# Optimization experiments

Measured on AMD Instinct MI355X. Metric: run time of the kernel, lower is better.

## Reference

```python
import jax, jax.numpy as jnp
import numpy as np

B, N, D = 32, 2048, 128
NUM_QUERIES = 16
K_FRAC = 0.5
NUM_SUPPORTS = N - NUM_QUERIES
K_KEEP = int(K_FRAC * NUM_SUPPORTS)  # 1016
M = K_KEEP + NUM_QUERIES             # pooled node count, 1032


def setup_inputs() -> dict:
    key = jax.random.key(0)
    k1, k2, k3 = jax.random.split(key, 3)
    A = jax.random.normal(k1, (B, N, N), dtype=jnp.float32)
    X = jax.random.normal(k2, (B, N, D), dtype=jnp.float32)
    w = jax.random.normal(k3, (D,), dtype=jnp.float32) * 0.1  # proj weight (out_dim=1)
    b = jnp.zeros((1,), dtype=jnp.float32)                     # proj bias
    return {"A": A, "X": X, "w": w, "b": b}


def reference(A, X, w, b):
    # per-node scores: sigmoid(Linear(X)/100), shape [B, N]
    scores = jax.nn.sigmoid((jnp.einsum('bnd,d->bn', X, w) + b[0]) / 100.0)
    support_scores = scores[:, :NUM_SUPPORTS]                     # [B, S]
    intra = support_scores - support_scores.mean(axis=1, keepdims=True)
    # torch.topk(largest=False) == top_k of negated values (ascending order)
    _, support_idx = jax.lax.top_k(-intra, K_KEEP)                # [B, K]
    support_values = jnp.take_along_axis(support_scores, support_idx, axis=1)
    query_idx = jnp.broadcast_to(jnp.arange(NUM_SUPPORTS, N, dtype=support_idx.dtype), (B, NUM_QUERIES))
    query_values = scores[:, NUM_SUPPORTS:]
    idx = jnp.concatenate([support_idx, query_idx], axis=1)       # [B, M]
    values = jnp.concatenate([support_values, query_values], axis=1)  # [B, M]
    # gather + scale node features
    new_X = jnp.take_along_axis(X, idx[:, :, None], axis=1) * values[:, :, None]  # [B, M, D]
    # double gather on adjacency: A[i, idx][:, idx]
    rows = jnp.take_along_axis(A, idx[:, :, None], axis=1)        # [B, M, N]
    new_A = jnp.take_along_axis(rows, idx[:, None, :], axis=2)    # [B, M, M]
    return (new_A, new_X, idx)
```

## Files before the change

kernel.cpp:

```cpp
#include <hip/hip_runtime.h>

#define NB 32
#define NN 2048
#define ND 128
#define NSUP 2032
#define KKEEP 1016
#define MM 1032
#define SEG 254

typedef unsigned long long u64;
typedef unsigned int u32;
typedef float f32x4 __attribute__((ext_vector_type(4)));

__device__ __forceinline__ float mulrn(float a, float b) {
  float r;
  asm("v_mul_f32 %0, %1, %2" : "=v"(r) : "v"(a), "v"(b));
  return r;
}
__device__ __forceinline__ float addrn(float a, float b) {
  float r;
  asm("v_add_f32 %0, %1, %2" : "=v"(r) : "v"(a), "v"(b));
  return r;
}
__device__ __forceinline__ float fmarn(float a, float b, float c) {
  float r;
  asm("v_fma_f32 %0, %1, %2, %3" : "=v"(r) : "v"(a), "v"(b), "v"(c));
  return r;
}

__global__ __launch_bounds__(256) void k_score(const float* __restrict__ X,
                                               const float* __restrict__ w,
                                               const float* __restrict__ bias,
                                               u64* __restrict__ keys,
                                               float* __restrict__ score) {
#pragma clang fp contract(off)
  int row = blockIdx.x * 256 + threadIdx.x;
  if (row >= NB * NN) return;
  const float* x = X + (size_t)row * ND;

  float l[16];
  #pragma unroll
  for (int k = 0; k < 16; ++k) l[k] = 0.f;
  #pragma unroll
  for (int step = 0; step < 8; ++step) {
    const float* xp = x + step * 16;
    const float* wp = w + step * 16;
    #pragma unroll
    for (int q4 = 0; q4 < 4; ++q4) {
      const float4 xv = *reinterpret_cast<const float4*>(xp + q4 * 4);
      const float4 wv = *reinterpret_cast<const float4*>(wp + q4 * 4);
      l[q4 * 4 + 0] = addrn(mulrn(xv.x, wv.x), l[q4 * 4 + 0]);
      l[q4 * 4 + 1] = addrn(mulrn(xv.y, wv.y), l[q4 * 4 + 1]);
      l[q4 * 4 + 2] = addrn(mulrn(xv.z, wv.z), l[q4 * 4 + 2]);
      l[q4 * 4 + 3] = addrn(mulrn(xv.w, wv.w), l[q4 * 4 + 3]);
    }
  }
  #pragma unroll
  for (int k = 0; k < 8; ++k) l[k] = addrn(l[k], l[k + 8]);
  #pragma unroll
  for (int k = 0; k < 4; ++k) l[k] = addrn(l[k], l[k + 4]);
  l[0] = addrn(l[0], l[2]);
  l[1] = addrn(l[1], l[3]);
  const float dot = addrn(l[0], l[1]);

  const float z = __fdiv_rn(addrn(dot, bias[0]), 100.0f);

  const float xe = -z;
  const float z2 = mulrn(xe, xe);
  float y = fmarn(1.9875691500E-4f, xe, 1.3981999507E-3f);
  y = fmarn(y, xe, 8.3334519073E-3f);
  y = fmarn(y, xe, 4.1665795894E-2f);
  y = fmarn(y, xe, 1.6666665459E-1f);
  y = fmarn(y, xe, 5.0000001201E-1f);
  y = fmarn(y, z2, xe);
  const float e = addrn(y, 1.0f);

  const float s = __fdiv_rn(1.0f, addrn(1.0f, e));

  score[row] = s;

  const u32 sb = __float_as_uint(s);
  const int n = row & (NN - 1);
  keys[row] = ((u64)sb << 32) | (u32)n;
}

__global__ __launch_bounds__(256) void k_rank(const u64* __restrict__ keys,
                                              const float* __restrict__ score,
                                              int* __restrict__ idxs,
                                              float* __restrict__ vals,
                                              float* __restrict__ out_idx) {
  __shared__ u64 lk[NSUP];
  const int b   = blockIdx.x >> 3;
  const int seg = blockIdx.x & 7;
  const int t   = threadIdx.x;
  const size_t bNN = (size_t)b * NN;
  const int    bMM = b * MM;

  for (int i = t; i < NSUP; i += 256) lk[i] = keys[bNN + i];
  __syncthreads();

  if (t < SEG) {
    const int e  = seg * SEG + t;
    const u64 my = lk[e];
    int cnt = 0;
    #pragma unroll 4
    for (int s = 0; s < NSUP; s += 4) {
      const u64 k0 = lk[s], k1 = lk[s + 1], k2 = lk[s + 2], k3 = lk[s + 3];
      cnt += (int)(k0 < my) + (int)(k1 < my) + (int)(k2 < my) + (int)(k3 < my);
    }
    if (cnt < KKEEP) {
      idxs[bMM + cnt]    = e;
      vals[bMM + cnt]    = score[bNN + e];
      out_idx[bMM + cnt] = (float)e;
    }
  } else {
    const int q   = seg * 2 + (t - SEG);
    const int e   = NSUP + q;
    const int pos = KKEEP + q;
    idxs[bMM + pos]    = e;
    vals[bMM + pos]    = score[bNN + e];
    out_idx[bMM + pos] = (float)e;
  }
}

__global__ __launch_bounds__(128) void k_newa(const float* __restrict__ A,
                                              const float* __restrict__ X,
                                              const int* __restrict__ idxs,
                                              const float* __restrict__ vals,
                                              float* __restrict__ out_a,
                                              float* __restrict__ out_x) {
  __shared__ float srow[NN];
  __shared__ int   scols[MM];
  int row = blockIdx.x;
  int b   = row / MM;
  const int* cols = idxs + b * MM;
  for (int c = threadIdx.x; c < MM / 4; c += 128)
    *reinterpret_cast<int4*>(&scols[c * 4]) =
        reinterpret_cast<const int4*>(cols)[c];

  int ri = idxs[row];
  const float* arow = A + ((size_t)b * NN + ri) * NN;
  #pragma unroll
  for (int i = 0; i < 4; ++i) {
    int off = (threadIdx.x + i * 128) * 4;
    *reinterpret_cast<f32x4*>(&srow[off]) =
        __builtin_nontemporal_load(reinterpret_cast<const f32x4*>(arow + off));
  }

  if (threadIdx.x < 32) {
    float v = vals[row];
    const float4 xv = reinterpret_cast<const float4*>(
        X + ((size_t)b * NN + ri) * ND)[threadIdx.x];
    float4 o = make_float4(xv.x * v, xv.y * v, xv.z * v, xv.w * v);
    reinterpret_cast<float4*>(out_x + (size_t)row * ND)[threadIdx.x] = o;
  }
  __syncthreads();

  f32x4* orow = reinterpret_cast<f32x4*>(out_a + (size_t)row * MM);
  for (int c = threadIdx.x; c < MM / 4; c += 128) {
    const int4 j4 = *reinterpret_cast<const int4*>(scols + c * 4);
    f32x4 o;
    o.x = srow[j4.x];
    o.y = srow[j4.y];
    o.z = srow[j4.z];
    o.w = srow[j4.w];
    __builtin_nontemporal_store(o, orow + c);
  }
}

extern "C" void kernel_launch(void* const* d_in, const int* in_sizes, int n_in,
                              void* d_out, int out_size, void* d_ws, size_t ws_size,
                              hipStream_t stream) {
  const float* A    = (const float*)d_in[0];
  const float* X    = (const float*)d_in[1];
  const float* w    = (const float*)d_in[2];
  const float* bias = (const float*)d_in[3];

  float* out0 = (float*)d_out;
  float* out1 = out0 + (size_t)NB * MM * MM;
  float* out2 = out1 + (size_t)NB * MM * ND;

  u64*   keys  = (u64*)d_ws;
  float* score = (float*)(keys + NB * NN);
  int*   idxs  = (int*)(score + NB * NN);
  float* vals  = (float*)(idxs + NB * MM);

  hipLaunchKernelGGL(k_score, dim3(NB * NN / 256), dim3(256), 0, stream, X, w, bias, keys, score);
  hipLaunchKernelGGL(k_rank,  dim3(NB * 8),        dim3(256), 0, stream, keys, score, idxs, vals, out2);
  hipLaunchKernelGGL(k_newa,  dim3(NB * MM),       dim3(128), 0, stream, A, X, idxs, vals, out0, out1);
}
```

Baseline: 109.8 us.

## Process multiple rows per block in k_newa with double-buffered row prefetch

The gather kernel now handles 12 output rows per 256-thread block instead of one row per 128-thread block. The column index table is loaded once per block and reused across those rows. The next source row of A is prefetched into registers while the current row is gathered from shared memory, with double-buffered LDS. This amortises per-block setup and overlaps the global load latency with the gather and store, at the cost of fewer blocks (2752) and two barriers per row.

After: 129.7 us. 1.18x slower.

```diff
diff --git a/kernel.cpp b/kernel.cpp
--- a/kernel.cpp
+++ b/kernel.cpp
@@ -7,6 +7,7 @@
 #define KKEEP 1016
 #define MM 1032
 #define SEG 254
+#define RPB 12
 
 typedef unsigned long long u64;
 typedef unsigned int u32;
@@ -123,48 +124,73 @@
   }
 }
 
-__global__ __launch_bounds__(128) void k_newa(const float* __restrict__ A,
+__global__ __launch_bounds__(256) void k_newa(const float* __restrict__ A,
                                               const float* __restrict__ X,
                                               const int* __restrict__ idxs,
                                               const float* __restrict__ vals,
                                               float* __restrict__ out_a,
                                               float* __restrict__ out_x) {
-  __shared__ float srow[NN];
+  __shared__ float buf[2][NN];
   __shared__ int   scols[MM];
-  int row = blockIdx.x;
-  int b   = row / MM;
+  const int t     = threadIdx.x;
+  const int b     = blockIdx.x / (MM / RPB);
+  const int chunk = blockIdx.x % (MM / RPB);
+  const int row0  = b * MM + chunk * RPB;
   const int* cols = idxs + b * MM;
-  for (int c = threadIdx.x; c < MM / 4; c += 128)
+  const float* Ab = A + (size_t)b * NN * NN;
+  const float* Xb = X + (size_t)b * NN * ND;
+
+  for (int c = t; c < MM / 4; c += 256)
     *reinterpret_cast<int4*>(&scols[c * 4]) =
         reinterpret_cast<const int4*>(cols)[c];
 
-  int ri = idxs[row];
-  const float* arow = A + ((size_t)b * NN + ri) * NN;
-  #pragma unroll
-  for (int i = 0; i < 4; ++i) {
-    int off = (threadIdx.x + i * 128) * 4;
-    *reinterpret_cast<f32x4*>(&srow[off]) =
-        __builtin_nontemporal_load(reinterpret_cast<const f32x4*>(arow + off));
-  }
-
-  if (threadIdx.x < 32) {
-    float v = vals[row];
-    const float4 xv = reinterpret_cast<const float4*>(
-        X + ((size_t)b * NN + ri) * ND)[threadIdx.x];
-    float4 o = make_float4(xv.x * v, xv.y * v, xv.z * v, xv.w * v);
-    reinterpret_cast<float4*>(out_x + (size_t)row * ND)[threadIdx.x] = o;
-  }
+  f32x4 r0, r1;
+  {
+    const f32x4* ar = reinterpret_cast<const f32x4*>(Ab + (size_t)idxs[row0] * NN);
+    r0 = __builtin_nontemporal_load(ar + t);
+    r1 = __builtin_nontemporal_load(ar + 256 + t);
+  }
+  reinterpret_cast<f32x4*>(buf[0])[t]       = r0;
+  reinterpret_cast<f32x4*>(buf[0])[256 + t] = r1;
   __syncthreads();
 
-  f32x4* orow = reinterpret_cast<f32x4*>(out_a + (size_t)row * MM);
-  for (int c = threadIdx.x; c < MM / 4; c += 128) {
-    const int4 j4 = *reinterpret_cast<const int4*>(scols + c * 4);
-    f32x4 o;
-    o.x = srow[j4.x];
-    o.y = srow[j4.y];
-    o.z = srow[j4.z];
-    o.w = srow[j4.w];
-    __builtin_nontemporal_store(o, orow + c);
+  int cur = 0;
+  for (int r = 0; r < RPB; ++r) {
+    const int row = row0 + r;
+    const bool more = (r + 1 < RPB);
+    if (more) {
+      const f32x4* ar = reinterpret_cast<const f32x4*>(
+          Ab + (size_t)idxs[row + 1] * NN);
+      r0 = __builtin_nontemporal_load(ar + t);
+      r1 = __builtin_nontemporal_load(ar + 256 + t);
+    }
+
+    if (t < 32) {
+      const float v = vals[row];
+      const float4 xv = reinterpret_cast<const float4*>(
+          Xb + (size_t)idxs[row] * ND)[t];
+      float4 o = make_float4(xv.x * v, xv.y * v, xv.z * v, xv.w * v);
+      reinterpret_cast<float4*>(out_x + (size_t)row * ND)[t] = o;
+    }
+
+    const float* sr = buf[cur];
+    f32x4* orow = reinterpret_cast<f32x4*>(out_a + (size_t)row * MM);
+    for (int c = t; c < MM / 4; c += 256) {
+      const int4 j4 = *reinterpret_cast<const int4*>(scols + c * 4);
+      f32x4 o;
+      o.x = sr[j4.x];
+      o.y = sr[j4.y];
+      o.z = sr[j4.z];
+      o.w = sr[j4.w];
+      __builtin_nontemporal_store(o, orow + c);
+    }
+    __syncthreads();
+    if (more) {
+      reinterpret_cast<f32x4*>(buf[cur ^ 1])[t]       = r0;
+      reinterpret_cast<f32x4*>(buf[cur ^ 1])[256 + t] = r1;
+    }
+    __syncthreads();
+    cur ^= 1;
   }
 }
 
@@ -185,7 +211,7 @@
   int*   idxs  = (int*)(score + NB * NN);
   float* vals  = (float*)(idxs + NB * MM);
 
-  hipLaunchKernelGGL(k_score, dim3(NB * NN / 256), dim3(256), 0, stream, X, w, bias, keys, score);
-  hipLaunchKernelGGL(k_rank,  dim3(NB * 8),        dim3(256), 0, stream, keys, score, idxs, vals, out2);
-  hipLaunchKernelGGL(k_newa,  dim3(NB * MM),       dim3(128), 0, stream, A, X, idxs, vals, out0, out1);
-}
+  hipLaunchKernelGGL(k_score, dim3(NB * NN / 256),    dim3(256), 0, stream, X, w, bias, keys, score);
+  hipLaunchKernelGGL(k_rank,  dim3(NB * 8),           dim3(256), 0, stream, keys, score, idxs, vals, out2);
+  hipLaunchKernelGGL(k_newa,  dim3(NB * (MM / RPB)),  dim3(256), 0, stream, A, X, idxs, vals, out0, out1);
+}
```
